# Kernel tuning notes

Hardware: AMD Instinct MI355X
Metric: run time of the kernel (lower is better)

## Reference

```python
import jax, jax.numpy as jnp
import numpy as np

B, C, T = 8, 512, 1024
EXP = 2
E = EXP * C          # 1024, gate/value width
H, HD = 8, 64        # heads, qk head dim
QK = H * HD          # 512
AVG_LEN = 512
EPS = 1e-5


def setup_inputs() -> dict:
    key = jax.random.key(0)
    ks = jax.random.split(key, 10)
    s = 0.02
    return {
        "x": jax.random.normal(ks[0], (B, C, T), jnp.float32),
        "W_in": jax.random.normal(ks[1], (2 * E, C), jnp.float32) * s,
        "b_in": jnp.zeros((2 * E,), jnp.float32),
        "W_attn": jax.random.normal(ks[2], (QK, C), jnp.float32) * s,
        "b_attn": jnp.zeros((QK,), jnp.float32),
        "w_q": 1.0 + jax.random.normal(ks[3], (QK,), jnp.float32) * 0.1,
        "b_q": jax.random.normal(ks[4], (QK,), jnp.float32) * 0.1,
        "w_k": 1.0 + jax.random.normal(ks[5], (QK,), jnp.float32) * 0.1,
        "b_k": jax.random.normal(ks[6], (QK,), jnp.float32) * 0.1,
        "W_out": jax.random.normal(ks[7], (C, E), jnp.float32) * s,
        "b_out": jnp.zeros((C,), jnp.float32),
        "gamma": jnp.ones((C,), jnp.float32),
    }


def reference(x, W_in, b_in, W_attn, b_attn, w_q, b_q, w_k, b_k, W_out, b_out, gamma):
    residual = x
    # mlp_in (1x1 conv) + SiLU, then chunk into gate u and value v, each (B,E,T)
    uv = jax.nn.silu(jnp.einsum('oc,bct->bot', W_in, x) + b_in[:, None])
    u, v = uv[:, :E], uv[:, E:]
    # mlp_attn (1x1 conv); no activation (activation_attn unused in forward)
    z = jnp.einsum('oc,bct->bot', W_attn, x) + b_attn[:, None]  # (B,QK,T)
    # depthwise 1x1 conv on cat(z,z) = two independent per-channel affines
    q = z * w_q[:, None] + b_q[:, None]
    k = z * w_k[:, None] + b_k[:, None]
    # split heads: q,k -> (B,H,T,HD); v -> (B,H,T,E//H)
    q = q.reshape(B, H, HD, T).transpose(0, 1, 3, 2)
    k = k.reshape(B, H, HD, T).transpose(0, 1, 3, 2)
    vh = v.reshape(B, H, E // H, T).transpose(0, 1, 3, 2)
    # entropy-invariant scale: (log n / log avg_len) / sqrt(d)
    scale = (np.log(T) / np.log(AVG_LEN)) / np.sqrt(HD)
    scores = jnp.einsum('bhqd,bhkd->bhqk', q, k) * jnp.float32(scale)
    attn = jax.nn.softmax(scores, axis=-1)
    o = jnp.einsum('bhqk,bhke->bhqe', attn, vh)        # (B,H,T,E//H)
    o = o.transpose(0, 1, 3, 2).reshape(B, E, T)       # back to (B,E,T)
    # gate, project out, residual + RMSNorm over channel dim
    out = jnp.einsum('ce,bet->bct', W_out, u * o) + b_out[:, None]
    y = residual + out
    rms = jax.lax.rsqrt(jnp.mean(y * y, axis=1, keepdims=True) + EPS)
    return y * rms * gamma[:, None]
```

## Files before the change

### kernel.cpp

```cpp
#include <hip/hip_runtime.h>

typedef __attribute__((ext_vector_type(8))) short short8;
typedef __attribute__((ext_vector_type(4))) float f32x4;
typedef __attribute__((ext_vector_type(16))) float f32x16;

__device__ __forceinline__ unsigned short f2b(float f) {
  union { float f; unsigned u; } x; x.f = f;
  unsigned r = (x.u + 0x7fffu + ((x.u >> 16) & 1u)) >> 16;
  return (unsigned short)r;
}
__device__ __forceinline__ float b2f(unsigned short b) {
  union { unsigned u; float f; } x; x.u = ((unsigned)b) << 16;
  return x.f;
}
__device__ __forceinline__ unsigned cvtpk(float lo, float hi) {
  unsigned r;
  asm("v_cvt_pk_bf16_f32 %0, %1, %2" : "=v"(r) : "v"(lo), "v"(hi));
  return r;
}
__device__ __forceinline__ void plswap(unsigned& a, unsigned& b) {
  asm volatile("v_permlane32_swap_b32 %0, %1" : "+v"(a), "+v"(b));
}

#define GLDS16(gp, lp)                                                                  \
  __builtin_amdgcn_global_load_lds((const __attribute__((address_space(1))) void*)(gp), \
                                   (__attribute__((address_space(3))) void*)(lp), 16, 0, 0)

__global__ void prep_w_kernel(const float* __restrict__ W_in, const float* __restrict__ W_attn,
                              const float* __restrict__ W_out, unsigned short* __restrict__ Wcat,
                              unsigned short* __restrict__ WoutB) {
  const int n1 = 2048 * 512, n2 = 512 * 512, n3 = 512 * 1024;
  for (int i = blockIdx.x * 256 + threadIdx.x; i < n1 + n2 + n3; i += gridDim.x * 256) {
    if (i < n1) Wcat[i] = f2b(W_in[i]);
    else if (i < n1 + n2) Wcat[i] = f2b(W_attn[i - n1]);
    else WoutB[i - n1 - n2] = f2b(W_out[i - n1 - n2]);
  }
}

__global__ __launch_bounds__(256) void transpose_x_kernel(const float* __restrict__ x,
                                                          unsigned short* __restrict__ xT) {
  __shared__ float tile[32][33];
  const int bid = blockIdx.x;
  const int b = bid & 7;
  const int rem = bid >> 3;
  const int c0 = (rem >> 5) << 5;
  const int t0 = (rem & 31) << 5;
  const int tj = threadIdx.x & 31, ti = threadIdx.x >> 5;
#pragma unroll
  for (int r = 0; r < 32; r += 8)
    tile[ti + r][tj] = x[(((size_t)b << 9) + c0 + ti + r) * 1024 + t0 + tj];
  __syncthreads();
#pragma unroll
  for (int r = 0; r < 32; r += 8)
    xT[(((size_t)b << 10) + t0 + ti + r) * 512 + c0 + tj] = f2b(tile[tj][ti + r]);
}

__device__ __forceinline__ void gemm_stage(const unsigned short* Ag, const unsigned short* Bg,
                                           int lda, int ldb, int k0, unsigned short* lsA,
                                           unsigned short* lsB, int buf, int sr, int sk,
                                           int ldst) {
  const int bb = buf * 8192;
  GLDS16(Ag + (size_t)sr * lda + k0 + sk, (char*)lsA + bb + ldst);
  GLDS16(Ag + (size_t)(sr + 64) * lda + k0 + sk, (char*)lsA + bb + 4096 + ldst);
  GLDS16(Bg + (size_t)sr * ldb + k0 + sk, (char*)lsB + bb + ldst);
  GLDS16(Bg + (size_t)(sr + 64) * ldb + k0 + sk, (char*)lsB + bb + 4096 + ldst);
}

__device__ __forceinline__ void gemm_bt_core(const unsigned short* __restrict__ Ag,
                                             const unsigned short* __restrict__ Bg, int lda,
                                             int ldb, int K, unsigned short* lsA,
                                             unsigned short* lsB, f32x4 acc[4][4]) {
  const int tid = threadIdx.x;
  const int lane = tid & 63;
  const int w = tid >> 6;
  const int wr = w >> 1, wc = w & 1;
  const int sr = tid >> 2;
  const int sk = (((tid & 3) ^ ((sr >> 1) & 3)) << 3);
  const int ldst = (tid >> 6) << 10;

  const int nt = K >> 5;
  int c0b = 0, c1b = 1, c2b = 2;
  gemm_stage(Ag, Bg, lda, ldb, 0, lsA, lsB, 0, sr, sk, ldst);
  gemm_stage(Ag, Bg, lda, ldb, 32, lsA, lsB, 1, sr, sk, ldst);
  for (int t = 0; t < nt; ++t) {
    if (t + 1 < nt) {
      asm volatile("s_waitcnt vmcnt(4)" ::: "memory");
    } else {
      asm volatile("s_waitcnt vmcnt(0)" ::: "memory");
    }
    __builtin_amdgcn_s_barrier();
    if (t + 2 < nt)
      gemm_stage(Ag, Bg, lda, ldb, (t + 2) << 5, lsA, lsB, c2b, sr, sk, ldst);
    short8 af[4], bfr[4];
    const int bb = c0b * 8192;
    const int ko = (lane >> 4) << 4;
    const int ra = (wr << 6) + (lane & 15);
    const int rb = (wc << 6) + (lane & 15);
#pragma unroll
    for (int mi = 0; mi < 4; ++mi) {
      const int rowA = ra + (mi << 4);
      af[mi] = *(const short8*)((const char*)lsA + bb + (rowA << 6) +
                                (ko ^ (((rowA >> 1) & 3) << 4)));
    }
#pragma unroll
    for (int ni = 0; ni < 4; ++ni) {
      const int rowB = rb + (ni << 4);
      bfr[ni] = *(const short8*)((const char*)lsB + bb + (rowB << 6) +
                                 (ko ^ (((rowB >> 1) & 3) << 4)));
    }
#pragma unroll
    for (int mi = 0; mi < 4; ++mi)
#pragma unroll
      for (int ni = 0; ni < 4; ++ni)
        acc[mi][ni] =
            __builtin_amdgcn_mfma_f32_16x16x32_bf16(af[mi], bfr[ni], acc[mi][ni], 0, 0, 0);
    const int tmp = c0b; c0b = c1b; c1b = c2b; c2b = tmp;
  }
}

__global__ __launch_bounds__(256) void gemm_a_kernel(
    const unsigned short* __restrict__ Wcat, const unsigned short* __restrict__ xT,
    const float* __restrict__ b_in, const float* __restrict__ b_attn,
    const float* __restrict__ w_q, const float* __restrict__ b_q, const float* __restrict__ w_k,
    const float* __restrict__ b_k, unsigned short* __restrict__ u, unsigned short* __restrict__ v,
    unsigned short* __restrict__ qT, unsigned short* __restrict__ kT) {
  __shared__ __align__(16) unsigned short lsA[12288];
  __shared__ __align__(16) unsigned short lsB[12288];
  const int bid = ((blockIdx.x & 7) * 160) + (blockIdx.x >> 3);
  const int b = bid / 160;
  const int rem = bid % 160;
  const int m0 = (rem >> 3) << 7;
  const int n0 = (rem & 7) << 7;
  f32x4 acc[4][4];
  const f32x4 z4 = {0.f, 0.f, 0.f, 0.f};
#pragma unroll
  for (int mi = 0; mi < 4; ++mi)
#pragma unroll
    for (int ni = 0; ni < 4; ++ni) acc[mi][ni] = z4;

  const unsigned short* Ag = Wcat + (size_t)m0 * 512;
  const unsigned short* Bg = xT + ((size_t)b << 19) + ((size_t)n0 << 9);
  gemm_bt_core(Ag, Bg, 512, 512, 512, lsA, lsB, acc);

  const int lane = threadIdx.x & 63;
  const int w = threadIdx.x >> 6;
  const int wr = w >> 1, wc = w & 1;
#pragma unroll
  for (int mi = 0; mi < 4; ++mi) {
    const int row0 = m0 + (wr << 6) + (mi << 4) + ((lane >> 4) << 2);
#pragma unroll
    for (int ni = 0; ni < 4; ++ni) {
      const int col = n0 + (wc << 6) + (ni << 4) + (lane & 15);
      if (row0 < 2048) {
#pragma unroll
        for (int i = 0; i < 4; ++i) {
          const int row = row0 + i;
          const float s = acc[mi][ni][i] + b_in[row];
          const float r = s / (1.f + __expf(-s));
          if (row < 1024)
            u[((((size_t)b << 10) + row) << 10) + col] = f2b(r);
          else
            v[((((size_t)b << 10) + (row - 1024)) << 10) + col] = f2b(r);
        }
      } else {
        const int c0 = row0 - 2048;
        ushort4 qv, kv;
        unsigned short* qp = (unsigned short*)&qv;
        unsigned short* kp = (unsigned short*)&kv;
#pragma unroll
        for (int i = 0; i < 4; ++i) {
          const int c = c0 + i;
          const float z = acc[mi][ni][i] + b_attn[c];
          qp[i] = f2b(z * w_q[c] + b_q[c]);
          kp[i] = f2b(z * w_k[c] + b_k[c]);
        }
        const int h = c0 >> 6, d = c0 & 63;
        const size_t base = ((((size_t)b * 8 + h) << 10) + col) * 64 + d;
        *(ushort4*)(qT + base) = qv;
        *(ushort4*)(kT + base) = kv;
      }
    }
  }
}

__global__ __launch_bounds__(256, 2) void attn_kernel(const unsigned short* __restrict__ qT,
                                                      const unsigned short* __restrict__ kT,
                                                      const unsigned short* __restrict__ v,
                                                      const unsigned short* __restrict__ u,
                                                      unsigned short* __restrict__ uoT) {
  __shared__ __align__(16) unsigned short Kls[3 * 4096];
  __shared__ __align__(16) unsigned short Vls[3 * 8192];
  const float SCALE2 = 0.20037430567f;
  const int bx = blockIdx.x;
  const int xcd = bx & 7, idx = bx >> 3;
  const int bh = (xcd << 3) + (idx & 7);
  const int qb = idx >> 3;
  const int b = bh >> 3, h = bh & 7;
  const int tid = threadIdx.x;
  const int lane = tid & 63;
  const int w = tid >> 6;
  const int l5 = lane >> 5;
  const int l31 = lane & 31;
  const int q0 = qb << 7;

  const unsigned short* qh = qT + ((size_t)bh << 16);
  const unsigned short* kh = kT + ((size_t)bh << 16);
  const unsigned short* vh = v + ((((size_t)b << 10) + (h << 7)) << 10);

  short8 qf[4];
#pragma unroll
  for (int ds = 0; ds < 4; ++ds)
    qf[ds] = *(const short8*)(qh + (size_t)(q0 + (w << 5) + l31) * 64 + (ds << 4) + (l5 << 3));

  f32x16 o[4];
#pragma unroll
  for (int eb = 0; eb < 4; ++eb)
#pragma unroll
    for (int i = 0; i < 16; ++i) o[eb][i] = 0.f;
  float lacc = 0.f;

  const int srow = tid >> 3;
  const int scol = (((tid & 7) ^ (srow & 7)) << 3);

#define ATTN_STAGE(buf, kt)                                                            \
  {                                                                                    \
    const int t2 = (kt) << 6;                                                          \
    char* kbase = (char*)Kls + (buf)*8192;                                             \
    char* vbase = (char*)Vls + (buf)*16384;                                            \
    GLDS16(kh + (size_t)(t2 + srow) * 64 + scol, kbase + (w << 10));                   \
    GLDS16(kh + (size_t)(t2 + 32 + srow) * 64 + scol, kbase + 4096 + (w << 10));       \
    GLDS16(vh + ((size_t)srow << 10) + t2 + scol, vbase + (w << 10));                  \
    GLDS16(vh + ((size_t)(32 + srow) << 10) + t2 + scol, vbase + 4096 + (w << 10));    \
    GLDS16(vh + ((size_t)(64 + srow) << 10) + t2 + scol, vbase + 8192 + (w << 10));    \
    GLDS16(vh + ((size_t)(96 + srow) << 10) + t2 + scol, vbase + 12288 + (w << 10));   \
  }

  int c0b = 0, c1b = 1, c2b = 2;
  ATTN_STAGE(0, 0);
  ATTN_STAGE(1, 1);
  union U8 { short8 s8; unsigned u4[4]; };
  for (int kt = 0; kt < 16; ++kt) {
    if (kt < 15) {
      asm volatile("s_waitcnt vmcnt(6)" ::: "memory");
    } else {
      asm volatile("s_waitcnt vmcnt(0)" ::: "memory");
    }
    __builtin_amdgcn_s_barrier();
    if (kt < 14) ATTN_STAGE(c2b, kt + 2);

    const char* kb = (const char*)Kls + c0b * 8192;
    const char* vb = (const char*)Vls + c0b * 16384;
    U8 pf[4];

    {
      f32x16 s;
#pragma unroll
      for (int i = 0; i < 16; ++i) s[i] = 0.f;
      const int kr = l31;
      __builtin_amdgcn_s_setprio(1);
#pragma unroll
      for (int ds = 0; ds < 4; ++ds) {
        short8 kf = *(const short8*)(kb + (kr << 7) +
                                     (((ds << 5) + (l5 << 4)) ^ ((kr & 7) << 4)));
        s = __builtin_amdgcn_mfma_f32_32x32x16_bf16(kf, qf[ds], s, 0, 0, 0);
      }
      __builtin_amdgcn_s_setprio(0);
      float p[16];
#pragma unroll
      for (int i = 0; i < 16; ++i) {
        p[i] = exp2f(s[i] * SCALE2);
        lacc += p[i];
      }
      unsigned W00 = cvtpk(p[0], p[1]), W01 = cvtpk(p[2], p[3]);
      unsigned W10 = cvtpk(p[4], p[5]), W11 = cvtpk(p[6], p[7]);
      unsigned W20 = cvtpk(p[8], p[9]), W21 = cvtpk(p[10], p[11]);
      unsigned W30 = cvtpk(p[12], p[13]), W31 = cvtpk(p[14], p[15]);
      unsigned a = W10, bq = W00; plswap(a, bq);
      pf[0].u4[0] = bq; pf[0].u4[2] = a;
      unsigned c = W11, d = W01; plswap(c, d);
      pf[0].u4[1] = d; pf[0].u4[3] = c;
      unsigned e = W30, f = W20; plswap(e, f);
      pf[1].u4[0] = f; pf[1].u4[2] = e;
      unsigned g = W31, hh = W21; plswap(g, hh);
      pf[1].u4[1] = hh; pf[1].u4[3] = g;
    }
    {
      f32x16 s;
#pragma unroll
      for (int i = 0; i < 16; ++i) s[i] = 0.f;
      const int kr = 32 + l31;
      __builtin_amdgcn_s_setprio(1);
#pragma unroll
      for (int ds = 0; ds < 4; ++ds) {
        short8 kf = *(const short8*)(kb + (kr << 7) +
                                     (((ds << 5) + (l5 << 4)) ^ ((kr & 7) << 4)));
        s = __builtin_amdgcn_mfma_f32_32x32x16_bf16(kf, qf[ds], s, 0, 0, 0);
      }
      __builtin_amdgcn_s_setprio(0);
      float p[16];
#pragma unroll
      for (int i = 0; i < 16; ++i) {
        p[i] = exp2f(s[i] * SCALE2);
        lacc += p[i];
      }
      unsigned W00 = cvtpk(p[0], p[1]), W01 = cvtpk(p[2], p[3]);
      unsigned W10 = cvtpk(p[4], p[5]), W11 = cvtpk(p[6], p[7]);
      unsigned W20 = cvtpk(p[8], p[9]), W21 = cvtpk(p[10], p[11]);
      unsigned W30 = cvtpk(p[12], p[13]), W31 = cvtpk(p[14], p[15]);
      unsigned a = W10, bq = W00; plswap(a, bq);
      pf[2].u4[0] = bq; pf[2].u4[2] = a;
      unsigned c = W11, d = W01; plswap(c, d);
      pf[2].u4[1] = d; pf[2].u4[3] = c;
      unsigned e = W30, f = W20; plswap(e, f);
      pf[3].u4[0] = f; pf[3].u4[2] = e;
      unsigned g = W31, hh = W21; plswap(g, hh);
      pf[3].u4[1] = hh; pf[3].u4[3] = g;
    }

    __builtin_amdgcn_s_setprio(1);
#pragma unroll
    for (int eb = 0; eb < 4; ++eb) {
      const int vrow = (eb << 5) + l31;
#pragma unroll
      for (int ks = 0; ks < 4; ++ks) {
        short8 vf = *(const short8*)(vb + (vrow << 7) +
                                     (((ks << 5) + (l5 << 4)) ^ ((vrow & 7) << 4)));
        o[eb] = __builtin_amdgcn_mfma_f32_32x32x16_bf16(vf, pf[ks].s8, o[eb], 0, 0, 0);
      }
    }
    __builtin_amdgcn_s_setprio(0);
    const int tmp = c0b; c0b = c1b; c1b = c2b; c2b = tmp;
  }
#undef ATTN_STAGE

  lacc += __shfl_xor(lacc, 32, 64);
  const float rl = 1.f / lacc;
  const int t = q0 + (w << 5) + l31;

#pragma unroll
  for (int eb = 0; eb < 4; ++eb) {
#pragma unroll
    for (int g = 0; g < 4; ++g) {
      const int e4 = (eb << 5) + (g << 3) + (l5 << 2);
      const int eg = (h << 7) + e4;
      ushort4 outv;
      unsigned short* op = (unsigned short*)&outv;
#pragma unroll
      for (int j = 0; j < 4; ++j) {
        const int i = (g << 2) + j;
        const float oo = o[eb][i] * rl;
        const float uu = b2f(u[((((size_t)b << 10) + eg + j) << 10) + t]);
        op[j] = f2b(oo * uu);
      }
      *(ushort4*)(uoT + ((((size_t)b << 10) + t) << 10) + eg) = outv;
    }
  }
}

__global__ __launch_bounds__(256) void gemm_c_kernel(const unsigned short* __restrict__ uoT,
                                                     const unsigned short* __restrict__ WoutB,
                                                     const float* __restrict__ x,
                                                     const float* __restrict__ b_out,
                                                     unsigned short* __restrict__ y) {
  __shared__ __align__(16) unsigned short lsA[12288];
  __shared__ __align__(16) unsigned short lsB[12288];
  const int bid = ((blockIdx.x & 7) * 32) + (blockIdx.x >> 3);
  const int b = bid >> 5;
  const int rem = bid & 31;
  const int m0 = (rem >> 2) << 7;
  const int n0 = (rem & 3) << 7;
  f32x4 acc[4][4];
  const f32x4 z4 = {0.f, 0.f, 0.f, 0.f};
#pragma unroll
  for (int mi = 0; mi < 4; ++mi)
#pragma unroll
    for (int ni = 0; ni < 4; ++ni) acc[mi][ni] = z4;

  const unsigned short* Ag = uoT + ((size_t)b << 20) + ((size_t)m0 << 10);
  const unsigned short* Bg = WoutB + ((size_t)n0 << 10);
  gemm_bt_core(Ag, Bg, 1024, 1024, 1024, lsA, lsB, acc);

  const int lane = threadIdx.x & 63;
  const int w = threadIdx.x >> 6;
  const int wr = w >> 1, wc = w & 1;
#pragma unroll
  for (int mi = 0; mi < 4; ++mi) {
    const int t4 = m0 + (wr << 6) + (mi << 4) + ((lane >> 4) << 2);
#pragma unroll
    for (int ni = 0; ni < 4; ++ni) {
      const int c = n0 + (wc << 6) + (ni << 4) + (lane & 15);
      const size_t base = ((((size_t)b << 9) + c) << 10) + t4;
      const f32x4 xv = *(const f32x4*)(x + base);
      const float bo = b_out[c];
      ushort4 ov;
      unsigned short* op = (unsigned short*)&ov;
#pragma unroll
      for (int i = 0; i < 4; ++i) op[i] = f2b(acc[mi][ni][i] + bo + xv[i]);
      *(ushort4*)(y + base) = ov;
    }
  }
}

__global__ __launch_bounds__(256) void rms_kernel(const unsigned short* __restrict__ y,
                                                  const float* __restrict__ gamma,
                                                  float* __restrict__ out) {
  __shared__ float part[8][32];
  __shared__ float rmsv[32];
  const int bid = blockIdx.x;
  const int b = bid >> 5;
  const int t0 = (bid & 31) << 5;
  const int tid = threadIdx.x;
  const int tt = tid & 31, cg = tid >> 5;
  const int t = t0 + tt;
  float vals[64];
  float ss = 0.f;
#pragma unroll
  for (int ci = 0; ci < 64; ++ci) {
    const int c = (cg << 6) + ci;
    const float vv = b2f(y[((((size_t)b << 9) + c) << 10) + t]);
    vals[ci] = vv;
    ss += vv * vv;
  }
  part[cg][tt] = ss;
  __syncthreads();
  if (tid < 32) {
    float tot = 0.f;
#pragma unroll
    for (int g = 0; g < 8; ++g) tot += part[g][tid];
    rmsv[tid] = rsqrtf(tot / 512.f + 1e-5f);
  }
  __syncthreads();
  const float rm = rmsv[tt];
#pragma unroll
  for (int ci = 0; ci < 64; ++ci) {
    const int c = (cg << 6) + ci;
    out[((((size_t)b << 9) + c) << 10) + t] = vals[ci] * rm * gamma[c];
  }
}

extern "C" void kernel_launch(void* const* d_in, const int* in_sizes, int n_in, void* d_out,
                              int out_size, void* d_ws, size_t ws_size, hipStream_t stream) {
  const float* x = (const float*)d_in[0];
  const float* W_in = (const float*)d_in[1];
  const float* b_in = (const float*)d_in[2];
  const float* W_attn = (const float*)d_in[3];
  const float* b_attn = (const float*)d_in[4];
  const float* w_q = (const float*)d_in[5];
  const float* b_q = (const float*)d_in[6];
  const float* w_k = (const float*)d_in[7];
  const float* b_k = (const float*)d_in[8];
  const float* W_out = (const float*)d_in[9];
  const float* b_out = (const float*)d_in[10];
  const float* gamma = (const float*)d_in[11];
  float* out = (float*)d_out;

  char* ws = (char*)d_ws;
  size_t off = 0;
  auto alloc = [&](size_t bytes) {
    char* p = ws + off;
    off += (bytes + 255) & ~(size_t)255;
    return p;
  };
  unsigned short* Wcat = (unsigned short*)alloc((size_t)2560 * 512 * 2);
  unsigned short* WoutB = (unsigned short*)alloc((size_t)512 * 1024 * 2);
  unsigned short* xT = (unsigned short*)alloc((size_t)8 * 1024 * 512 * 2);
  unsigned short* u = (unsigned short*)alloc((size_t)8 * 1024 * 1024 * 2);
  unsigned short* v = (unsigned short*)alloc((size_t)8 * 1024 * 1024 * 2);
  unsigned short* qT = (unsigned short*)alloc((size_t)8 * 8 * 1024 * 64 * 2);
  unsigned short* kT = (unsigned short*)alloc((size_t)8 * 8 * 1024 * 64 * 2);
  unsigned short* uoT = (unsigned short*)alloc((size_t)8 * 1024 * 1024 * 2);
  unsigned short* y = (unsigned short*)alloc((size_t)8 * 512 * 1024 * 2);
  if (off > ws_size) return;

  prep_w_kernel<<<896, 256, 0, stream>>>(W_in, W_attn, W_out, Wcat, WoutB);
  transpose_x_kernel<<<4096, 256, 0, stream>>>(x, xT);
  gemm_a_kernel<<<1280, 256, 0, stream>>>(Wcat, xT, b_in, b_attn, w_q, b_q, w_k, b_k, u, v, qT,
                                          kT);
  attn_kernel<<<512, 256, 0, stream>>>(qT, kT, v, u, uoT);
  gemm_c_kernel<<<256, 256, 0, stream>>>(uoT, WoutB, x, b_out, y);
  rms_kernel<<<256, 256, 0, stream>>>(y, gamma, out);
}
```

Baseline: 124.0 us.

## Software-pipeline attention QK and PV MFMAs and merge prep kernels

Restructures the attention inner loop so the QK^T score MFMAs for tile kt are interleaved with the PV MFMAs for tile kt-1, using probabilities packed in the previous iteration. This lets exp/pack work and matrix ops from different tiles overlap instead of serialising QK, softmax and PV within one tile. The buffer rotation changes to separate K and V buffer indices and adds an extra barrier before refilling the freed buffer. Separately, the weight-conversion and x-transpose kernels are fused into one launch to save a kernel launch. The pipelined loop raises register pressure, since prior-tile probabilities and all K fragments stay live.

```diff
diff --git a/kernel.cpp b/kernel.cpp
--- a/kernel.cpp
+++ b/kernel.cpp
@@ -26,33 +26,36 @@
   __builtin_amdgcn_global_load_lds((const __attribute__((address_space(1))) void*)(gp), \
                                    (__attribute__((address_space(3))) void*)(lp), 16, 0, 0)
 
-__global__ void prep_w_kernel(const float* __restrict__ W_in, const float* __restrict__ W_attn,
-                              const float* __restrict__ W_out, unsigned short* __restrict__ Wcat,
-                              unsigned short* __restrict__ WoutB) {
-  const int n1 = 2048 * 512, n2 = 512 * 512, n3 = 512 * 1024;
-  for (int i = blockIdx.x * 256 + threadIdx.x; i < n1 + n2 + n3; i += gridDim.x * 256) {
-    if (i < n1) Wcat[i] = f2b(W_in[i]);
-    else if (i < n1 + n2) Wcat[i] = f2b(W_attn[i - n1]);
-    else WoutB[i - n1 - n2] = f2b(W_out[i - n1 - n2]);
-  }
-}
-
-__global__ __launch_bounds__(256) void transpose_x_kernel(const float* __restrict__ x,
-                                                          unsigned short* __restrict__ xT) {
-  __shared__ float tile[32][33];
-  const int bid = blockIdx.x;
-  const int b = bid & 7;
-  const int rem = bid >> 3;
-  const int c0 = (rem >> 5) << 5;
-  const int t0 = (rem & 31) << 5;
-  const int tj = threadIdx.x & 31, ti = threadIdx.x >> 5;
-#pragma unroll
-  for (int r = 0; r < 32; r += 8)
-    tile[ti + r][tj] = x[(((size_t)b << 9) + c0 + ti + r) * 1024 + t0 + tj];
-  __syncthreads();
-#pragma unroll
-  for (int r = 0; r < 32; r += 8)
-    xT[(((size_t)b << 10) + t0 + ti + r) * 512 + c0 + tj] = f2b(tile[tj][ti + r]);
+__global__ __launch_bounds__(256) void prep_kernel(const float* __restrict__ x,
+                                                   const float* __restrict__ W_in,
+                                                   const float* __restrict__ W_attn,
+                                                   const float* __restrict__ W_out,
+                                                   unsigned short* __restrict__ Wcat,
+                                                   unsigned short* __restrict__ WoutB,
+                                                   unsigned short* __restrict__ xT) {
+  if (blockIdx.x < 4096) {
+    __shared__ float tile[32][33];
+    const int bid = blockIdx.x;
+    const int b = bid & 7;
+    const int rem = bid >> 3;
+    const int c0 = (rem >> 5) << 5;
+    const int t0 = (rem & 31) << 5;
+    const int tj = threadIdx.x & 31, ti = threadIdx.x >> 5;
+#pragma unroll
+    for (int r = 0; r < 32; r += 8)
+      tile[ti + r][tj] = x[(((size_t)b << 9) + c0 + ti + r) * 1024 + t0 + tj];
+    __syncthreads();
+#pragma unroll
+    for (int r = 0; r < 32; r += 8)
+      xT[(((size_t)b << 10) + t0 + ti + r) * 512 + c0 + tj] = f2b(tile[tj][ti + r]);
+  } else {
+    const int n1 = 2048 * 512, n2 = 512 * 512, n3 = 512 * 1024;
+    for (int i = (blockIdx.x - 4096) * 256 + threadIdx.x; i < n1 + n2 + n3; i += 896 * 256) {
+      if (i < n1) Wcat[i] = f2b(W_in[i]);
+      else if (i < n1 + n2) Wcat[i] = f2b(W_attn[i - n1]);
+      else WoutB[i - n1 - n2] = f2b(W_out[i - n1 - n2]);
+    }
+  }
 }
 
 __device__ __forceinline__ void gemm_stage(const unsigned short* Ag, const unsigned short* Bg,
@@ -235,103 +238,131 @@
     GLDS16(vh + ((size_t)(96 + srow) << 10) + t2 + scol, vbase + 12288 + (w << 10));   \
   }
 
-  int c0b = 0, c1b = 1, c2b = 2;
+#define KREAD(kbp, kr, ds)                                                             \
+  (*(const short8*)((kbp) + ((kr) << 7) + ((((ds) << 5) + (l5 << 4)) ^ (((kr)&7) << 4))))
+#define VREAD(vbp, vrow, ks)                                                           \
+  (*(const short8*)((vbp) + ((vrow) << 7) + ((((ks) << 5) + (l5 << 4)) ^ (((vrow)&7) << 4))))
+
+#define PACK(sv, out0, out1)                                                           \
+  do {                                                                                 \
+    float p_[16];                                                                      \
+    _Pragma("unroll") for (int i_ = 0; i_ < 16; ++i_) {                                \
+      p_[i_] = exp2f(sv[i_] * SCALE2);                                                 \
+      lacc += p_[i_];                                                                  \
+    }                                                                                  \
+    unsigned W00 = cvtpk(p_[0], p_[1]), W01 = cvtpk(p_[2], p_[3]);                     \
+    unsigned W10 = cvtpk(p_[4], p_[5]), W11 = cvtpk(p_[6], p_[7]);                     \
+    unsigned W20 = cvtpk(p_[8], p_[9]), W21 = cvtpk(p_[10], p_[11]);                   \
+    unsigned W30 = cvtpk(p_[12], p_[13]), W31 = cvtpk(p_[14], p_[15]);                 \
+    unsigned a_ = W10, b_ = W00;                                                       \
+    plswap(a_, b_);                                                                    \
+    (out0).u4[0] = b_; (out0).u4[2] = a_;                                              \
+    unsigned c_ = W11, d_ = W01;                                                       \
+    plswap(c_, d_);                                                                    \
+    (out0).u4[1] = d_; (out0).u4[3] = c_;                                              \
+    unsigned e_ = W30, f_ = W20;                                                       \
+    plswap(e_, f_);                                                                    \
+    (out1).u4[0] = f_; (out1).u4[2] = e_;                                              \
+    unsigned g_ = W31, h_ = W21;                                                       \
+    plswap(g_, h_);                                                                    \
+    (out1).u4[1] = h_; (out1).u4[3] = g_;                                              \
+  } while (0)
+
+  union U8 { short8 s8; unsigned u4[4]; };
+  U8 pfP[4];
+
   ATTN_STAGE(0, 0);
   ATTN_STAGE(1, 1);
-  union U8 { short8 s8; unsigned u4[4]; };
-  for (int kt = 0; kt < 16; ++kt) {
+
+  asm volatile("s_waitcnt vmcnt(6)" ::: "memory");
+  __builtin_amdgcn_s_barrier();
+  {
+    const char* kb = (const char*)Kls;
+    f32x16 s0, s1;
+#pragma unroll
+    for (int i = 0; i < 16; ++i) { s0[i] = 0.f; s1[i] = 0.f; }
+    __builtin_amdgcn_s_setprio(1);
+#pragma unroll
+    for (int ds = 0; ds < 4; ++ds) {
+      short8 kfA = KREAD(kb, l31, ds);
+      s0 = __builtin_amdgcn_mfma_f32_32x32x16_bf16(kfA, qf[ds], s0, 0, 0, 0);
+      short8 kfB = KREAD(kb, 32 + l31, ds);
+      s1 = __builtin_amdgcn_mfma_f32_32x32x16_bf16(kfB, qf[ds], s1, 0, 0, 0);
+    }
+    __builtin_amdgcn_s_setprio(0);
+    PACK(s0, pfP[0], pfP[1]);
+    PACK(s1, pfP[2], pfP[3]);
+  }
+  __builtin_amdgcn_s_barrier();
+  ATTN_STAGE(2, 2);
+
+  int ck = 1, cv = 0;
+  for (int kt = 1; kt < 16; ++kt) {
     if (kt < 15) {
       asm volatile("s_waitcnt vmcnt(6)" ::: "memory");
     } else {
       asm volatile("s_waitcnt vmcnt(0)" ::: "memory");
     }
     __builtin_amdgcn_s_barrier();
-    if (kt < 14) ATTN_STAGE(c2b, kt + 2);
-
-    const char* kb = (const char*)Kls + c0b * 8192;
-    const char* vb = (const char*)Vls + c0b * 16384;
-    U8 pf[4];
-
-    {
-      f32x16 s;
-#pragma unroll
-      for (int i = 0; i < 16; ++i) s[i] = 0.f;
-      const int kr = l31;
-      __builtin_amdgcn_s_setprio(1);
-#pragma unroll
-      for (int ds = 0; ds < 4; ++ds) {
-        short8 kf = *(const short8*)(kb + (kr << 7) +
-                                     (((ds << 5) + (l5 << 4)) ^ ((kr & 7) << 4)));
-        s = __builtin_amdgcn_mfma_f32_32x32x16_bf16(kf, qf[ds], s, 0, 0, 0);
+
+    const char* kb = (const char*)Kls + ck * 8192;
+    const char* vb = (const char*)Vls + cv * 16384;
+
+    short8 kfA[4], kfB[4];
+#pragma unroll
+    for (int ds = 0; ds < 4; ++ds) {
+      kfA[ds] = KREAD(kb, l31, ds);
+      kfB[ds] = KREAD(kb, 32 + l31, ds);
+    }
+
+    f32x16 s0, s1;
+#pragma unroll
+    for (int i = 0; i < 16; ++i) { s0[i] = 0.f; s1[i] = 0.f; }
+    __builtin_amdgcn_s_setprio(1);
+#pragma unroll
+    for (int ks = 0; ks < 4; ++ks) {
+      s0 = __builtin_amdgcn_mfma_f32_32x32x16_bf16(kfA[ks], qf[ks], s0, 0, 0, 0);
+      s1 = __builtin_amdgcn_mfma_f32_32x32x16_bf16(kfB[ks], qf[ks], s1, 0, 0, 0);
+#pragma unroll
+      for (int eb = 0; eb < 4; ++eb) {
+        short8 vf = VREAD(vb, (eb << 5) + l31, ks);
+        o[eb] = __builtin_amdgcn_mfma_f32_32x32x16_bf16(vf, pfP[ks].s8, o[eb], 0, 0, 0);
       }
-      __builtin_amdgcn_s_setprio(0);
-      float p[16];
-#pragma unroll
-      for (int i = 0; i < 16; ++i) {
-        p[i] = exp2f(s[i] * SCALE2);
-        lacc += p[i];
+    }
+    __builtin_amdgcn_s_setprio(0);
+
+    U8 pfN[4];
+    PACK(s0, pfN[0], pfN[1]);
+    PACK(s1, pfN[2], pfN[3]);
+#pragma unroll
+    for (int i = 0; i < 4; ++i) pfP[i] = pfN[i];
+
+    if (kt + 2 < 16) {
+      __builtin_amdgcn_s_barrier();
+      ATTN_STAGE(cv, kt + 2);
+    }
+    const int third = 3 - ck - cv;
+    cv = ck;
+    ck = third;
+  }
+
+  {
+    const char* vb = (const char*)Vls + cv * 16384;
+    __builtin_amdgcn_s_setprio(1);
+#pragma unroll
+    for (int ks = 0; ks < 4; ++ks) {
+#pragma unroll
+      for (int eb = 0; eb < 4; ++eb) {
+        short8 vf = VREAD(vb, (eb << 5) + l31, ks);
+        o[eb] = __builtin_amdgcn_mfma_f32_32x32x16_bf16(vf, pfP[ks].s8, o[eb], 0, 0, 0);
       }
-      unsigned W00 = cvtpk(p[0], p[1]), W01 = cvtpk(p[2], p[3]);
-      unsigned W10 = cvtpk(p[4], p[5]), W11 = cvtpk(p[6], p[7]);
-      unsigned W20 = cvtpk(p[8], p[9]), W21 = cvtpk(p[10], p[11]);
-      unsigned W30 = cvtpk(p[12], p[13]), W31 = cvtpk(p[14], p[15]);
-      unsigned a = W10, bq = W00; plswap(a, bq);
-      pf[0].u4[0] = bq; pf[0].u4[2] = a;
-      unsigned c = W11, d = W01; plswap(c, d);
-      pf[0].u4[1] = d; pf[0].u4[3] = c;
-      unsigned e = W30, f = W20; plswap(e, f);
-      pf[1].u4[0] = f; pf[1].u4[2] = e;
-      unsigned g = W31, hh = W21; plswap(g, hh);
-      pf[1].u4[1] = hh; pf[1].u4[3] = g;
-    }
-    {
-      f32x16 s;
-#pragma unroll
-      for (int i = 0; i < 16; ++i) s[i] = 0.f;
-      const int kr = 32 + l31;
-      __builtin_amdgcn_s_setprio(1);
-#pragma unroll
-      for (int ds = 0; ds < 4; ++ds) {
-        short8 kf = *(const short8*)(kb + (kr << 7) +
-                                     (((ds << 5) + (l5 << 4)) ^ ((kr & 7) << 4)));
-        s = __builtin_amdgcn_mfma_f32_32x32x16_bf16(kf, qf[ds], s, 0, 0, 0);
-      }
-      __builtin_amdgcn_s_setprio(0);
-      float p[16];
-#pragma unroll
-      for (int i = 0; i < 16; ++i) {
-        p[i] = exp2f(s[i] * SCALE2);
-        lacc += p[i];
-      }
-      unsigned W00 = cvtpk(p[0], p[1]), W01 = cvtpk(p[2], p[3]);
-      unsigned W10 = cvtpk(p[4], p[5]), W11 = cvtpk(p[6], p[7]);
-      unsigned W20 = cvtpk(p[8], p[9]), W21 = cvtpk(p[10], p[11]);
-      unsigned W30 = cvtpk(p[12], p[13]), W31 = cvtpk(p[14], p[15]);
-      unsigned a = W10, bq = W00; plswap(a, bq);
-      pf[2].u4[0] = bq; pf[2].u4[2] = a;
-      unsigned c = W11, d = W01; plswap(c, d);
-      pf[2].u4[1] = d; pf[2].u4[3] = c;
-      unsigned e = W30, f = W20; plswap(e, f);
-      pf[3].u4[0] = f; pf[3].u4[2] = e;
-      unsigned g = W31, hh = W21; plswap(g, hh);
-      pf[3].u4[1] = hh; pf[3].u4[3] = g;
-    }
-
-    __builtin_amdgcn_s_setprio(1);
-#pragma unroll
-    for (int eb = 0; eb < 4; ++eb) {
-      const int vrow = (eb << 5) + l31;
-#pragma unroll
-      for (int ks = 0; ks < 4; ++ks) {
-        short8 vf = *(const short8*)(vb + (vrow << 7) +
-                                     (((ks << 5) + (l5 << 4)) ^ ((vrow & 7) << 4)));
-        o[eb] = __builtin_amdgcn_mfma_f32_32x32x16_bf16(vf, pf[ks].s8, o[eb], 0, 0, 0);
-      }
     }
     __builtin_amdgcn_s_setprio(0);
-    const int tmp = c0b; c0b = c1b; c1b = c2b; c2b = tmp;
   }
 #undef ATTN_STAGE
+#undef KREAD
+#undef VREAD
+#undef PACK
 
   lacc += __shfl_xor(lacc, 32, 64);
   const float rl = 1.f / lacc;
@@ -472,8 +503,7 @@
   unsigned short* y = (unsigned short*)alloc((size_t)8 * 512 * 1024 * 2);
   if (off > ws_size) return;
 
-  prep_w_kernel<<<896, 256, 0, stream>>>(W_in, W_attn, W_out, Wcat, WoutB);
-  transpose_x_kernel<<<4096, 256, 0, stream>>>(x, xT);
+  prep_kernel<<<4992, 256, 0, stream>>>(x, W_in, W_attn, W_out, Wcat, WoutB, xT);
   gemm_a_kernel<<<1280, 256, 0, stream>>>(Wcat, xT, b_in, b_attn, w_q, b_q, w_k, b_k, u, v, qT,
                                           kT);
   attn_kernel<<<512, 256, 0, stream>>>(qT, kT, v, u, uoT);
```

New measurement: 121.0 us (median of 4 runs). -2.4%, faster.
